# Performance work log

Measured on AMD Instinct MI355X. Metric: run time of the kernel, lower is better.

Reference implementation:

```python
import jax, jax.numpy as jnp
import numpy as np

DIM_MODEL = 1024
NUM_HEADS = 16
DROPOUT_P = 0.5
SCALE = float(np.sqrt(DIM_MODEL // NUM_HEADS))  # NOTE: source MULTIPLIES by this (unusual but faithful)
DROP_KEY = jax.random.key(42)


def setup_inputs() -> dict:
    key = jax.random.key(0)
    ks = jax.random.split(key, 9)
    B, LQ, LK, D = 4, 2048, 2048, DIM_MODEL
    s = 1.0 / np.sqrt(D)
    return {
        "query": jax.random.normal(ks[0], (B, LQ, D), jnp.float32),
        "key": jax.random.normal(ks[1], (B, LK, D), jnp.float32),
        "value": jax.random.normal(ks[2], (B, LK, D), jnp.float32),
        "Wq": jax.random.normal(ks[3], (D, D), jnp.float32) * s,
        "bq": jax.random.normal(ks[4], (D,), jnp.float32) * s,
        "Wk": jax.random.normal(ks[5], (D, D), jnp.float32) * s,
        "bk": jax.random.normal(ks[6], (D,), jnp.float32) * s,
        "Wv": jax.random.normal(ks[7], (D, D), jnp.float32) * s,
        "bv": jax.random.normal(ks[8], (D,), jnp.float32) * s,
    }


def reference(query, key, value, Wq, bq, Wk, bk, Wv, bv):
    # Linear projections (W stored as [in, out])
    q = jnp.einsum('bqd,de->bqe', query, Wq) + bq
    k = jnp.einsum('bkd,de->bke', key, Wk) + bk
    v = jnp.einsum('bkd,de->bke', value, Wv) + bv
    # scores scaled by MULTIPLYING sqrt(d_head), per source
    scores = jnp.einsum('bqe,bke->bqk', q, k) * SCALE
    probs = jax.nn.softmax(scores, axis=-1)
    # dropout (train mode, p=0.5), deterministic fixed key for reproducibility
    keep = jax.random.bernoulli(DROP_KEY, 1.0 - DROPOUT_P, probs.shape)
    probs = jnp.where(keep, probs / (1.0 - DROPOUT_P), 0.0)
    return jnp.einsum('bqk,bke->bqe', probs, v)
```

## Files before the change

### kernel.cpp

```cpp
#include <hip/hip_runtime.h>
#include <math.h>

#define BATCH  4
#define LSEQ   2048
#define DMODEL 1024
#define MROWS  (BATCH * LSEQ)
#define SCORE_SCALE 8.0f

#define THREEFRY_PARTITIONABLE 1

typedef __bf16 bf16_t;
typedef bf16_t bf16x8 __attribute__((ext_vector_type(8)));
typedef bf16_t bf16x4 __attribute__((ext_vector_type(4)));
typedef float  f32x4  __attribute__((ext_vector_type(4)));

#define LDSP(p) ((__attribute__((address_space(3))) void*)(p))
#define GLBP(p) ((const __attribute__((address_space(1))) void*)(p))

__device__ __forceinline__ unsigned rotl32(unsigned x, int r) {
    return (x << r) | (x >> (32 - r));
}

__device__ __forceinline__ void threefry2x32(unsigned k0, unsigned k1,
                                             unsigned x0, unsigned x1,
                                             unsigned& o0, unsigned& o1) {
    const unsigned ks0 = k0, ks1 = k1, ks2 = k0 ^ k1 ^ 0x1BD11BDAu;
    x0 += ks0; x1 += ks1;
#define TF_R(r) { x0 += x1; x1 = rotl32(x1, r); x1 ^= x0; }
    TF_R(13) TF_R(15) TF_R(26) TF_R(6)
    x0 += ks1; x1 += ks2 + 1u;
    TF_R(17) TF_R(29) TF_R(16) TF_R(24)
    x0 += ks2; x1 += ks0 + 2u;
    TF_R(13) TF_R(15) TF_R(26) TF_R(6)
    x0 += ks0; x1 += ks1 + 3u;
    TF_R(17) TF_R(29) TF_R(16) TF_R(24)
    x0 += ks1; x1 += ks2 + 4u;
    TF_R(13) TF_R(15) TF_R(26) TF_R(6)
    x0 += ks2; x1 += ks0 + 5u;
#undef TF_R
    o0 = x0; o1 = x1;
}

__device__ __forceinline__ bool dropout_keep(unsigned n) {
    unsigned o0, o1;
#if THREEFRY_PARTITIONABLE
    threefry2x32(0u, 42u, 0u, n, o0, o1);
    unsigned bits = o0 ^ o1;
#else
    const unsigned HALF = (unsigned)(BATCH * LSEQ) * (unsigned)LSEQ / 2u;
    unsigned c0 = (n < HALF) ? n : (n - HALF);
    unsigned c1 = (n < HALF) ? (n + HALF) : n;
    threefry2x32(0u, 42u, c0, c1, o0, o1);
    unsigned bits = (n < HALF) ? o0 : o1;
#endif
    return bits < 0x80000000u;
}

__global__ __launch_bounds__(256)
void split_f32(const float* __restrict__ X0, const float* __restrict__ X1,
               bf16_t* __restrict__ hi, bf16_t* __restrict__ lo, int n) {
    const int y = blockIdx.y;
    const float* X = y ? X1 : X0;
    long long i = (long long)(blockIdx.x * 256 + threadIdx.x) * 4;
    if (i >= n) return;
    float4 v = *(const float4*)(X + i);
    bf16x4 h, l;
    h[0] = (bf16_t)v.x; l[0] = (bf16_t)(v.x - (float)h[0]);
    h[1] = (bf16_t)v.y; l[1] = (bf16_t)(v.y - (float)h[1]);
    h[2] = (bf16_t)v.z; l[2] = (bf16_t)(v.z - (float)h[2]);
    h[3] = (bf16_t)v.w; l[3] = (bf16_t)(v.w - (float)h[3]);
    *(bf16x4*)(hi + (long long)y * n + i) = h;
    *(bf16x4*)(lo + (long long)y * n + i) = l;
}

__global__ __launch_bounds__(256)
void cvt_bf16(const float* __restrict__ X, bf16_t* __restrict__ Y, int n) {
    long long i = (long long)(blockIdx.x * 256 + threadIdx.x) * 8;
    if (i >= n) return;
    float4 a = *(const float4*)(X + i);
    float4 b = *(const float4*)(X + i + 4);
    bf16x8 o;
    o[0] = (bf16_t)a.x; o[1] = (bf16_t)a.y; o[2] = (bf16_t)a.z; o[3] = (bf16_t)a.w;
    o[4] = (bf16_t)b.x; o[5] = (bf16_t)b.y; o[6] = (bf16_t)b.z; o[7] = (bf16_t)b.w;
    *(bf16x8*)(Y + i) = o;
}

__global__ __launch_bounds__(256)
void split_transpose(const float* __restrict__ W0, const float* __restrict__ W1,
                     bf16_t* __restrict__ Th, bf16_t* __restrict__ Tl,
                     int Kd, int Nd) {
    __shared__ float t[32][33];
    const int z = blockIdx.z;
    const float* W = z ? W1 : W0;
    const long long zo = (long long)z * Kd * Nd;
    const int bx = blockIdx.x * 32;
    const int by = blockIdx.y * 32;
    const int tx = threadIdx.x & 31, ty = threadIdx.x >> 5;
#pragma unroll
    for (int i = 0; i < 4; ++i)
        t[ty + i * 8][tx] = W[(long long)(by + ty + i * 8) * Nd + bx + tx];
    __syncthreads();
#pragma unroll
    for (int i = 0; i < 4; ++i) {
        float v = t[tx][ty + i * 8];
        long long idx = zo + (long long)(bx + ty + i * 8) * Kd + by + tx;
        bf16_t h = (bf16_t)v;
        Th[idx] = h;
        Tl[idx] = (bf16_t)(v - (float)h);
    }
}

template <int OUT>
__global__ __launch_bounds__(512, 2)
void gemm_pipe(const bf16_t* __restrict__ A, const bf16_t* __restrict__ B,
               const float* __restrict__ bias,
               float* __restrict__ Cf, bf16_t* __restrict__ Ch,
               int M, int N, int K, float scale,
               long long sA, long long sB, long long sC,
               int NYt, int NZ) {
    constexpr int ABUF = 128 * 32;
    constexpr int BUFE = ABUF + 256 * 32;
    __shared__ __align__(16) bf16_t smem[3 * BUFE];

    const int bid = blockIdx.x;
    const int gid = (bid & 7) * 32 + (bid >> 3);
    const int nzy = NZ * NYt;
    const int nx = gid / nzy;
    const int rem = gid - nx * nzy;
    const int zz = rem / NYt;
    const int my = rem - zz * NYt;
    const long long z = zz;
    const int m0 = my * 128, n0 = nx * 256;

    const int tid = threadIdx.x;
    const int lane = tid & 63;
    const int wave = tid >> 6;
    const int quad = lane >> 4;
    const int l16 = lane & 15;
    const int wm = (wave >> 2) * 64;
    const int wn = (wave & 3) * 64;

    const bf16_t* gA = A + z * sA;
    const bf16_t* gB = B + z * sB;

    const int lrow = lane >> 2;
    const int scol = ((lane & 3) ^ ((lrow >> 1) & 3)) * 8;
    const int sw = (l16 >> 1) & 3;

    auto stage_tile = [&](int k0, bf16_t* base) {
        {
            const int row = (wave << 4) + lrow;
            __builtin_amdgcn_global_load_lds(
                GLBP(gA + (long long)(m0 + row) * K + k0 + scol),
                LDSP(base + row * 32), 16, 0, 0);
        }
#pragma unroll
        for (int r = 0; r < 2; ++r) {
            const int row = (r << 7) + (wave << 4) + lrow;
            __builtin_amdgcn_global_load_lds(
                GLBP(gB + (long long)(n0 + row) * K + k0 + scol),
                LDSP(base + ABUF + row * 32), 16, 0, 0);
        }
    };

    f32x4 acc[4][4];
#pragma unroll
    for (int i = 0; i < 4; ++i)
#pragma unroll
        for (int j = 0; j < 4; ++j)
            acc[i][j] = (f32x4){0.f, 0.f, 0.f, 0.f};

    bf16x8 fa0[4], fb0[4], fa1[4], fb1[4];

    const int NIT = K >> 5;

    bf16_t* p0 = smem;
    bf16_t* p1 = smem + BUFE;
    bf16_t* p2 = smem + 2 * BUFE;

    stage_tile(0, p0);
    stage_tile(32, p1);
    stage_tile(64, p2);
    asm volatile("s_waitcnt vmcnt(3)" ::: "memory");
    asm volatile("s_barrier" ::: "memory");
    __builtin_amdgcn_sched_barrier(0);
#pragma unroll
    for (int i = 0; i < 4; ++i) {
        const int ao = (wm + i * 16 + l16) * 32 + (quad ^ sw) * 8;
        fa0[i] = *(const bf16x8*)(p0 + ao);
    }
#pragma unroll
    for (int j = 0; j < 4; ++j) {
        const int bo = ABUF + (wn + j * 16 + l16) * 32 + (quad ^ sw) * 8;
        fb0[j] = *(const bf16x8*)(p0 + bo);
    }

#define PIPE_ITER(T, FAc, FBc, FAn, FBn)                                      \
    {                                                                         \
        const int t_ = (T);                                                   \
        if (t_ + 1 < NIT) {                                                   \
            _Pragma("unroll")                                                 \
            for (int i = 0; i < 4; ++i) {                                     \
                const int ao = (wm + i * 16 + l16) * 32 + (quad ^ sw) * 8;    \
                FAn[i] = *(const bf16x8*)(p1 + ao);                           \
            }                                                                 \
            _Pragma("unroll")                                                 \
            for (int j = 0; j < 4; ++j) {                                     \
                const int bo = ABUF + (wn + j * 16 + l16) * 32 + (quad ^ sw) * 8; \
                FBn[j] = *(const bf16x8*)(p1 + bo);                           \
            }                                                                 \
        }                                                                     \
        if (t_ + 3 < NIT) stage_tile((t_ + 3) << 5, p0);                      \
        __builtin_amdgcn_s_setprio(1);                                        \
        _Pragma("unroll")                                                     \
        for (int i = 0; i < 4; ++i)                                           \
            _Pragma("unroll")                                                 \
            for (int j = 0; j < 4; ++j)                                       \
                acc[i][j] = __builtin_amdgcn_mfma_f32_16x16x32_bf16(          \
                    FAc[i], FBc[j], acc[i][j], 0, 0, 0);                      \
        __builtin_amdgcn_s_setprio(0);                                        \
        if (t_ + 2 < NIT) {                                                   \
            asm volatile("s_waitcnt lgkmcnt(0)" ::: "memory");                \
            if (t_ + 3 < NIT) asm volatile("s_waitcnt vmcnt(3)" ::: "memory");\
            else              asm volatile("s_waitcnt vmcnt(0)" ::: "memory");\
            asm volatile("s_barrier" ::: "memory");                           \
            __builtin_amdgcn_sched_barrier(0);                                \
        }                                                                     \
        { bf16_t* tmp_ = p0; p0 = p1; p1 = p2; p2 = tmp_; }                   \
    }

    for (int tp = 0; tp < NIT; tp += 2) {
        PIPE_ITER(tp,     fa0, fb0, fa1, fb1)
        PIPE_ITER(tp + 1, fa1, fb1, fa0, fb0)
    }
#undef PIPE_ITER

#pragma unroll
    for (int i = 0; i < 4; ++i)
#pragma unroll
        for (int j = 0; j < 4; ++j) {
            const int n = n0 + wn + j * 16 + l16;
#pragma unroll
            for (int r = 0; r < 4; ++r) {
                const int m = m0 + wm + i * 16 + quad * 4 + r;
                const long long idx = z * sC + (long long)m * N + n;
                float v = acc[i][j][r];
                if constexpr (OUT == 0) {
                    Cf[idx] = v * scale;
                } else {
                    Ch[idx] = (bf16_t)(v + bias[m]);
                }
            }
        }
}

template <int OUT>
__global__ __launch_bounds__(512, 2)
void gemm_mfma_8ph(const bf16_t* __restrict__ Ah, const bf16_t* __restrict__ Al,
                   const bf16_t* __restrict__ Bh, const bf16_t* __restrict__ Bl,
                   const float* __restrict__ bias, const float* __restrict__ bias2,
                   float* __restrict__ Cf, bf16_t* __restrict__ Ch,
                   bf16_t* __restrict__ Cl,
                   int M, int N, int K, float scale,
                   long long sA, long long sB, long long sC,
                   int NYt, int NZ) {
    constexpr int TM = 256, TN = 256;
    constexpr int PLANE = 256 * 32;
    constexpr int HB = 4 * PLANE;
    __shared__ __align__(16) bf16_t smem[2 * HB];

    const int bid = blockIdx.x;
    const int gid = (bid & 7) * 32 + (bid >> 3);
    const int nzy = NZ * NYt;
    const int nx = gid / nzy;
    const int rem = gid - nx * nzy;
    const int zz = rem / NYt;
    const int my = rem - zz * NYt;
    const long long z = zz;
    const int m0 = my * TM, n0 = nx * TN;

    const int tid = threadIdx.x;
    const int lane = tid & 63;
    const int wave = tid >> 6;
    const int quad = lane >> 4;
    const int l16 = lane & 15;
    const int wm = (wave >> 2) * 128;
    const int wn = (wave & 3) * 64;

    const bf16_t* gAh = Ah + z * sA;
    const bf16_t* gAl = Al + z * sA;
    const bf16_t* gBh = Bh + z * sB;
    const bf16_t* gBl = Bl + z * sB;

    const int lrow = lane >> 2;
    const int scol = ((lane & 3) ^ ((lrow >> 1) & 3)) * 8;
    const int sw = (l16 >> 1) & 3;

    auto stage_round = [&](int r, int k0, bf16_t* base) {
        if (r < 4) {
            const int row = ((r & 1) << 7) + (wave << 4) + lrow;
            const bf16_t* src = (r >= 2) ? gBl : gBh;
            bf16_t* dst = base + ((r >= 2) ? 3 : 2) * PLANE + row * 32;
            __builtin_amdgcn_global_load_lds(
                GLBP(src + (long long)(n0 + row) * K + k0 + scol), LDSP(dst), 16, 0, 0);
        } else {
            const int p = r - 4;
            const int row = (p << 5) + ((wave & 2) ? 128 : 0) + ((wave & 1) << 4) + lrow;
            const bf16_t* src = (wave >= 4) ? gAl : gAh;
            bf16_t* dst = base + ((wave >= 4) ? 1 : 0) * PLANE + row * 32;
            __builtin_amdgcn_global_load_lds(
                GLBP(src + (long long)(m0 + row) * K + k0 + scol), LDSP(dst), 16, 0, 0);
        }
    };

    f32x4 acc[8][4];
#pragma unroll
    for (int i = 0; i < 8; ++i)
#pragma unroll
        for (int j = 0; j < 4; ++j)
            acc[i][j] = (f32x4){0.f, 0.f, 0.f, 0.f};

    bf16x8 ah[2][2], al[2][2];
    bf16x8 bfh[4], bfl[4];

#pragma unroll
    for (int r = 0; r < 8; ++r) stage_round(r, 0, smem);
    asm volatile("s_waitcnt vmcnt(2)" ::: "memory");
    asm volatile("s_barrier" ::: "memory");
    __builtin_amdgcn_sched_barrier(0);
#pragma unroll
    for (int i = 0; i < 2; ++i) {
        const int ao = (wm + i * 16 + l16) * 32 + (quad ^ sw) * 8;
        ah[0][i] = *(const bf16x8*)(smem + ao);
        al[0][i] = *(const bf16x8*)(smem + PLANE + ao);
    }
#pragma unroll
    for (int j = 0; j < 4; ++j) {
        const int bo = (wn + j * 16 + l16) * 32 + (quad ^ sw) * 8;
        bfh[j] = *(const bf16x8*)(smem + 2 * PLANE + bo);
        bfl[j] = *(const bf16x8*)(smem + 3 * PLANE + bo);
    }

    const int NIT = K >> 5;
    for (int itp = 0; itp < NIT; itp += 2) {
#pragma unroll
        for (int h = 0; h < 2; ++h) {
            const int it = itp + h;
            const bool more = (it + 1) < NIT;
            const int k1 = (it + 1) << 5;
            bf16_t* cur = smem + h * HB;
            bf16_t* nxt = smem + (h ^ 1) * HB;
#pragma unroll
            for (int ph = 0; ph < 4; ++ph) {
                if (ph < 3) {
#pragma unroll
                    for (int i = 0; i < 2; ++i) {
                        const int ao = (wm + ((ph + 1) * 2 + i) * 16 + l16) * 32 + (quad ^ sw) * 8;
                        ah[(ph + 1) & 1][i] = *(const bf16x8*)(cur + ao);
                        al[(ph + 1) & 1][i] = *(const bf16x8*)(cur + PLANE + ao);
                    }
                } else if (more) {
#pragma unroll
                    for (int i = 0; i < 2; ++i) {
                        const int ao = (wm + i * 16 + l16) * 32 + (quad ^ sw) * 8;
                        ah[0][i] = *(const bf16x8*)(nxt + ao);
                        al[0][i] = *(const bf16x8*)(nxt + PLANE + ao);
                    }
                }
                if (more) {
                    if (ph == 0)      { stage_round(0, k1, nxt); stage_round(1, k1, nxt); stage_round(2, k1, nxt); }
                    else if (ph == 1) { stage_round(3, k1, nxt); stage_round(4, k1, nxt); }
                    else if (ph == 2) { stage_round(5, k1, nxt); stage_round(6, k1, nxt); }
                    else              { stage_round(7, k1, nxt); }
                }
                __builtin_amdgcn_s_setprio(1);
#pragma unroll
                for (int i = 0; i < 2; ++i)
#pragma unroll
                    for (int j = 0; j < 4; ++j) {
                        f32x4 a = acc[ph * 2 + i][j];
                        a = __builtin_amdgcn_mfma_f32_16x16x32_bf16(ah[ph & 1][i], bfh[j], a, 0, 0, 0);
                        a = __builtin_amdgcn_mfma_f32_16x16x32_bf16(ah[ph & 1][i], bfl[j], a, 0, 0, 0);
                        a = __builtin_amdgcn_mfma_f32_16x16x32_bf16(al[ph & 1][i], bfh[j], a, 0, 0, 0);
                        acc[ph * 2 + i][j] = a;
                    }
                __builtin_amdgcn_s_setprio(0);
                if (ph == 3 && more) {
#pragma unroll
                    for (int j = 0; j < 4; ++j) {
                        const int bo = (wn + j * 16 + l16) * 32 + (quad ^ sw) * 8;
                        bfh[j] = *(const bf16x8*)(nxt + 2 * PLANE + bo);
                        bfl[j] = *(const bf16x8*)(nxt + 3 * PLANE + bo);
                    }
                }
                if (more) {
                    if (ph == 0)      asm volatile("s_waitcnt vmcnt(4)" ::: "memory");
                    else if (ph == 1) asm volatile("s_waitcnt vmcnt(5)" ::: "memory");
                    else              asm volatile("s_waitcnt vmcnt(2)" ::: "memory");
                    asm volatile("s_barrier" ::: "memory");
                    __builtin_amdgcn_sched_barrier(0);
                } else {
                    if (ph == 0) {
                        asm volatile("s_waitcnt vmcnt(1)" ::: "memory");
                        asm volatile("s_barrier" ::: "memory");
                        __builtin_amdgcn_sched_barrier(0);
                    } else if (ph == 1) {
                        asm volatile("s_waitcnt vmcnt(0)" ::: "memory");
                        asm volatile("s_barrier" ::: "memory");
                        __builtin_amdgcn_sched_barrier(0);
                    }
                }
            }
        }
    }

    const float* bz = (z == 1 && bias2) ? bias2 : bias;
#pragma unroll
    for (int i = 0; i < 8; ++i)
#pragma unroll
        for (int j = 0; j < 4; ++j) {
            const int n = n0 + wn + j * 16 + l16;
            float bvn = 0.f;
            if constexpr (OUT != 0) bvn = bz[n];
#pragma unroll
            for (int r = 0; r < 4; ++r) {
                const int m = m0 + wm + i * 16 + quad * 4 + r;
                const long long idx = z * sC + (long long)m * N + n;
                float v = acc[i][j][r];
                if constexpr (OUT == 0) {
                    Cf[idx] = v * scale;
                } else {
                    v += bvn;
                    bf16_t h = (bf16_t)v;
                    Ch[idx] = h;
                    Cl[idx] = (bf16_t)(v - (float)h);
                }
            }
        }
}

__global__ __launch_bounds__(256)
void softmax_dropout(const float* __restrict__ S, bf16_t* __restrict__ P) {
    const unsigned row = blockIdx.x;
    const float* rp = S + (long long)row * LSEQ;
    const int tid = threadIdx.x;

    float v[8];
    *(float4*)(v)     = *(const float4*)(rp + tid * 8);
    *(float4*)(v + 4) = *(const float4*)(rp + tid * 8 + 4);

    float m = v[0];
#pragma unroll
    for (int e = 1; e < 8; ++e) m = fmaxf(m, v[e]);
#pragma unroll
    for (int o = 1; o < 64; o <<= 1) m = fmaxf(m, __shfl_xor(m, o));
    __shared__ float redm[4];
    if ((tid & 63) == 0) redm[tid >> 6] = m;
    __syncthreads();
    m = fmaxf(fmaxf(redm[0], redm[1]), fmaxf(redm[2], redm[3]));

    float s = 0.f;
#pragma unroll
    for (int e = 0; e < 8; ++e) { v[e] = __expf(v[e] - m); s += v[e]; }
#pragma unroll
    for (int o = 1; o < 64; o <<= 1) s += __shfl_xor(s, o);
    __shared__ float reds[4];
    if ((tid & 63) == 0) reds[tid >> 6] = s;
    __syncthreads();
    s = (reds[0] + reds[1]) + (reds[2] + reds[3]);

    const float inv = 2.0f / s;
    const unsigned nb = row * (unsigned)LSEQ + (unsigned)(tid * 8);
    bf16x8 o8;
#pragma unroll
    for (int e = 0; e < 8; ++e)
        o8[e] = (bf16_t)(dropout_keep(nb + e) ? v[e] * inv : 0.0f);
    *(bf16x8*)(P + (long long)row * LSEQ + tid * 8) = o8;
}

extern "C" void kernel_launch(void* const* d_in, const int* in_sizes, int n_in,
                              void* d_out, int out_size, void* d_ws, size_t ws_size,
                              hipStream_t stream) {
    const float* query = (const float*)d_in[0];
    const float* key_  = (const float*)d_in[1];
    const float* value = (const float*)d_in[2];
    const float* Wq = (const float*)d_in[3];
    const float* bq = (const float*)d_in[4];
    const float* Wk = (const float*)d_in[5];
    const float* bk = (const float*)d_in[6];
    const float* Wv = (const float*)d_in[7];
    const float* bv = (const float*)d_in[8];
    float* out = (float*)d_out;

    char* w = (char*)d_ws;
    const size_t Q1 = (size_t)MROWS * DMODEL * 2;
    bf16_t* Qh  = (bf16_t*)(w);
    bf16_t* Ql  = (bf16_t*)(w + 2 * Q1);
    bf16_t* VT  = (bf16_t*)(w + 4 * Q1);
    float*  S   = (float*)(w + 5 * Q1);
    bf16_t* XvH  = (bf16_t*)(w + 5 * Q1);
    bf16_t* XqkH = (bf16_t*)(w + 5 * Q1);
    bf16_t* XqkL = (bf16_t*)(w + 7 * Q1);
    bf16_t* WTh = (bf16_t*)(w + 9 * Q1);
    bf16_t* WTl = (bf16_t*)(w + 9 * Q1 + 2 * (size_t)DMODEL * DMODEL * 2);
    bf16_t* P   = Qh;

    dim3 b256(256);
    dim3 b512(512);
    const int NELEM = MROWS * DMODEL;
    const long long DD = (long long)DMODEL * DMODEL;
    dim3 gwt1(DMODEL / 32, DMODEL / 32, 1);
    dim3 gwt2(DMODEL / 32, DMODEL / 32, 2);

    split_transpose<<<gwt1, b256, 0, stream>>>(Wv, nullptr, WTh, WTl, DMODEL, DMODEL);
    cvt_bf16<<<dim3(NELEM / 2048), b256, 0, stream>>>(value, XvH, NELEM);
    gemm_pipe<2><<<dim3(256), b512, 0, stream>>>(
        WTh, XvH, bv, nullptr, VT,
        DMODEL, LSEQ, DMODEL, 1.f,
        0, (long long)LSEQ * DMODEL, (long long)DMODEL * LSEQ,
        DMODEL / 128, 4);

    split_transpose<<<gwt2, b256, 0, stream>>>(Wq, Wk, WTh, WTl, DMODEL, DMODEL);
    split_f32<<<dim3(NELEM / 1024, 2), b256, 0, stream>>>(query, key_, XqkH, XqkL, NELEM);
    gemm_mfma_8ph<1><<<dim3(256), b512, 0, stream>>>(
        XqkH, XqkL, WTh, WTl, bq, bk, nullptr, Qh, Ql,
        MROWS, DMODEL, DMODEL, 1.f,
        (long long)NELEM, DD, (long long)NELEM,
        MROWS / 256, 2);

    gemm_mfma_8ph<0><<<dim3(256), b512, 0, stream>>>(
        Qh, Ql, Qh + NELEM, Ql + NELEM, nullptr, nullptr, S, nullptr, nullptr,
        LSEQ, LSEQ, DMODEL, SCORE_SCALE,
        (long long)LSEQ * DMODEL, (long long)LSEQ * DMODEL,
        (long long)LSEQ * LSEQ,
        LSEQ / 256, 4);

    softmax_dropout<<<dim3(MROWS), b256, 0, stream>>>(S, P);

    gemm_pipe<0><<<dim3(256), b512, 0, stream>>>(
        P, VT, nullptr, out, nullptr,
        LSEQ, DMODEL, LSEQ, 1.f,
        (long long)LSEQ * LSEQ, (long long)DMODEL * LSEQ, (long long)LSEQ * DMODEL,
        LSEQ / 128, 4);
}
```

Baseline: 425.1 us.

## Stage GEMM epilogues through LDS for vectorized stores and merge prep kernels

GEMM epilogues now write each wave's accumulator tile into a swizzled LDS strip, then read it back as rows so global stores are 4-wide contiguous vectors instead of scattered scalar stores. This targets the uncoalesced writes of the large S score matrix and of the Q/K hi/lo outputs. Separately, the weight split/transpose and input conversion kernels for Q, K and V are fused into two launches, which requires rearranging workspace buffers so they do not alias. The fused launches add an extra LDS round trip and barrier per epilogue and bring a risk of buffer overlap errors.

```diff
diff --git a/kernel.cpp b/kernel.cpp
--- a/kernel.cpp
+++ b/kernel.cpp
@@ -57,10 +57,12 @@
 }
 
 __global__ __launch_bounds__(256)
-void split_f32(const float* __restrict__ X0, const float* __restrict__ X1,
-               bf16_t* __restrict__ hi, bf16_t* __restrict__ lo, int n) {
+void split_all(const float* __restrict__ Xq, const float* __restrict__ Xk,
+               const float* __restrict__ Xv,
+               bf16_t* __restrict__ hi, bf16_t* __restrict__ lo,
+               bf16_t* __restrict__ vh, int n) {
     const int y = blockIdx.y;
-    const float* X = y ? X1 : X0;
+    const float* X = (y == 0) ? Xq : (y == 1) ? Xk : Xv;
     long long i = (long long)(blockIdx.x * 256 + threadIdx.x) * 4;
     if (i >= n) return;
     float4 v = *(const float4*)(X + i);
@@ -69,30 +71,25 @@
     h[1] = (bf16_t)v.y; l[1] = (bf16_t)(v.y - (float)h[1]);
     h[2] = (bf16_t)v.z; l[2] = (bf16_t)(v.z - (float)h[2]);
     h[3] = (bf16_t)v.w; l[3] = (bf16_t)(v.w - (float)h[3]);
-    *(bf16x4*)(hi + (long long)y * n + i) = h;
-    *(bf16x4*)(lo + (long long)y * n + i) = l;
+    if (y < 2) {
+        *(bf16x4*)(hi + (long long)y * n + i) = h;
+        *(bf16x4*)(lo + (long long)y * n + i) = l;
+    } else {
+        *(bf16x4*)(vh + i) = h;
+    }
 }
 
 __global__ __launch_bounds__(256)
-void cvt_bf16(const float* __restrict__ X, bf16_t* __restrict__ Y, int n) {
-    long long i = (long long)(blockIdx.x * 256 + threadIdx.x) * 8;
-    if (i >= n) return;
-    float4 a = *(const float4*)(X + i);
-    float4 b = *(const float4*)(X + i + 4);
-    bf16x8 o;
-    o[0] = (bf16_t)a.x; o[1] = (bf16_t)a.y; o[2] = (bf16_t)a.z; o[3] = (bf16_t)a.w;
-    o[4] = (bf16_t)b.x; o[5] = (bf16_t)b.y; o[6] = (bf16_t)b.z; o[7] = (bf16_t)b.w;
-    *(bf16x8*)(Y + i) = o;
-}
-
-__global__ __launch_bounds__(256)
-void split_transpose(const float* __restrict__ W0, const float* __restrict__ W1,
-                     bf16_t* __restrict__ Th, bf16_t* __restrict__ Tl,
-                     int Kd, int Nd) {
+void split_transpose3(const float* __restrict__ W0, const float* __restrict__ W1,
+                      const float* __restrict__ W2,
+                      bf16_t* __restrict__ Th01, bf16_t* __restrict__ Tl01,
+                      bf16_t* __restrict__ Thv, bf16_t* __restrict__ Tlv,
+                      int Kd, int Nd) {
     __shared__ float t[32][33];
     const int z = blockIdx.z;
-    const float* W = z ? W1 : W0;
-    const long long zo = (long long)z * Kd * Nd;
+    const float* W = (z == 0) ? W0 : (z == 1) ? W1 : W2;
+    bf16_t* Th = (z == 2) ? Thv : Th01 + (long long)z * Kd * Nd;
+    bf16_t* Tl = (z == 2) ? Tlv : Tl01 + (long long)z * Kd * Nd;
     const int bx = blockIdx.x * 32;
     const int by = blockIdx.y * 32;
     const int tx = threadIdx.x & 31, ty = threadIdx.x >> 5;
@@ -103,7 +100,7 @@
 #pragma unroll
     for (int i = 0; i < 4; ++i) {
         float v = t[tx][ty + i * 8];
-        long long idx = zo + (long long)(bx + ty + i * 8) * Kd + by + tx;
+        long long idx = (long long)(bx + ty + i * 8) * Kd + by + tx;
         bf16_t h = (bf16_t)v;
         Th[idx] = h;
         Tl[idx] = (bf16_t)(v - (float)h);
@@ -235,23 +232,43 @@
     }
 #undef PIPE_ITER
 
-#pragma unroll
-    for (int i = 0; i < 4; ++i)
-#pragma unroll
-        for (int j = 0; j < 4; ++j) {
-            const int n = n0 + wn + j * 16 + l16;
+    asm volatile("s_barrier" ::: "memory");
+    float* strip = (float*)smem + wave * 1024;
+#pragma unroll
+    for (int i = 0; i < 4; ++i) {
+#pragma unroll
+        for (int j = 0; j < 4; ++j)
 #pragma unroll
             for (int r = 0; r < 4; ++r) {
-                const int m = m0 + wm + i * 16 + quad * 4 + r;
-                const long long idx = z * sC + (long long)m * N + n;
-                float v = acc[i][j][r];
-                if constexpr (OUT == 0) {
-                    Cf[idx] = v * scale;
-                } else {
-                    Ch[idx] = (bf16_t)(v + bias[m]);
-                }
+                const int row = quad * 4 + r;
+                const int col = j * 16 + l16;
+                strip[row * 64 + (col ^ (row << 2))] = acc[i][j][r];
+            }
+        asm volatile("s_waitcnt lgkmcnt(0)" ::: "memory");
+        __builtin_amdgcn_sched_barrier(0);
+#pragma unroll
+        for (int k = 0; k < 4; ++k) {
+            const int R = k * 4 + (lane >> 4);
+            const int c = (lane & 15) * 4;
+            f32x4 v = *(const f32x4*)(strip + R * 64 + (c ^ (R << 2)));
+            const int grow = m0 + wm + i * 16 + R;
+            const int gcol = n0 + wn + c;
+            const long long idx = z * sC + (long long)grow * N + gcol;
+            if constexpr (OUT == 0) {
+                v *= scale;
+                *(f32x4*)(Cf + idx) = v;
+            } else {
+                const float bm = bias[grow];
+                v += bm;
+                bf16x4 h4;
+                h4[0] = (bf16_t)v[0]; h4[1] = (bf16_t)v[1];
+                h4[2] = (bf16_t)v[2]; h4[3] = (bf16_t)v[3];
+                *(bf16x4*)(Ch + idx) = h4;
             }
         }
+        asm volatile("s_waitcnt lgkmcnt(0)" ::: "memory");
+        __builtin_amdgcn_sched_barrier(0);
+    }
 }
 
 template <int OUT>
@@ -414,29 +431,48 @@
         }
     }
 
+    asm volatile("s_barrier" ::: "memory");
+    float* strip = (float*)smem + wave * 1024;
     const float* bz = (z == 1 && bias2) ? bias2 : bias;
 #pragma unroll
-    for (int i = 0; i < 8; ++i)
-#pragma unroll
-        for (int j = 0; j < 4; ++j) {
-            const int n = n0 + wn + j * 16 + l16;
-            float bvn = 0.f;
-            if constexpr (OUT != 0) bvn = bz[n];
+    for (int i = 0; i < 8; ++i) {
+#pragma unroll
+        for (int j = 0; j < 4; ++j)
 #pragma unroll
             for (int r = 0; r < 4; ++r) {
-                const int m = m0 + wm + i * 16 + quad * 4 + r;
-                const long long idx = z * sC + (long long)m * N + n;
-                float v = acc[i][j][r];
-                if constexpr (OUT == 0) {
-                    Cf[idx] = v * scale;
-                } else {
-                    v += bvn;
-                    bf16_t h = (bf16_t)v;
-                    Ch[idx] = h;
-                    Cl[idx] = (bf16_t)(v - (float)h);
+                const int row = quad * 4 + r;
+                const int col = j * 16 + l16;
+                strip[row * 64 + (col ^ (row << 2))] = acc[i][j][r];
+            }
+        asm volatile("s_waitcnt lgkmcnt(0)" ::: "memory");
+        __builtin_amdgcn_sched_barrier(0);
+#pragma unroll
+        for (int k = 0; k < 4; ++k) {
+            const int R = k * 4 + (lane >> 4);
+            const int c = (lane & 15) * 4;
+            f32x4 v = *(const f32x4*)(strip + R * 64 + (c ^ (R << 2)));
+            const int grow = m0 + wm + i * 16 + R;
+            const int gcol = n0 + wn + c;
+            const long long idx = z * sC + (long long)grow * N + gcol;
+            if constexpr (OUT == 0) {
+                v *= scale;
+                *(f32x4*)(Cf + idx) = v;
+            } else {
+                f32x4 b4 = *(const f32x4*)(bz + gcol);
+                v += b4;
+                bf16x4 h4, l4;
+#pragma unroll
+                for (int e = 0; e < 4; ++e) {
+                    h4[e] = (bf16_t)v[e];
+                    l4[e] = (bf16_t)(v[e] - (float)h4[e]);
                 }
+                *(bf16x4*)(Ch + idx) = h4;
+                *(bf16x4*)(Cl + idx) = l4;
             }
         }
+        asm volatile("s_waitcnt lgkmcnt(0)" ::: "memory");
+        __builtin_amdgcn_sched_barrier(0);
+    }
 }
 
 __global__ __launch_bounds__(256)
@@ -494,11 +530,14 @@
 
     char* w = (char*)d_ws;
     const size_t Q1 = (size_t)MROWS * DMODEL * 2;
+    const long long DD = (long long)DMODEL * DMODEL;
     bf16_t* Qh  = (bf16_t*)(w);
     bf16_t* Ql  = (bf16_t*)(w + 2 * Q1);
     bf16_t* VT  = (bf16_t*)(w + 4 * Q1);
     float*  S   = (float*)(w + 5 * Q1);
-    bf16_t* XvH  = (bf16_t*)(w + 5 * Q1);
+    bf16_t* XvH  = (bf16_t*)(w);
+    bf16_t* WvTh = (bf16_t*)(w + 2 * Q1);
+    bf16_t* WvTl = WvTh + DD;
     bf16_t* XqkH = (bf16_t*)(w + 5 * Q1);
     bf16_t* XqkL = (bf16_t*)(w + 7 * Q1);
     bf16_t* WTh = (bf16_t*)(w + 9 * Q1);
@@ -508,20 +547,18 @@
     dim3 b256(256);
     dim3 b512(512);
     const int NELEM = MROWS * DMODEL;
-    const long long DD = (long long)DMODEL * DMODEL;
-    dim3 gwt1(DMODEL / 32, DMODEL / 32, 1);
-    dim3 gwt2(DMODEL / 32, DMODEL / 32, 2);
-
-    split_transpose<<<gwt1, b256, 0, stream>>>(Wv, nullptr, WTh, WTl, DMODEL, DMODEL);
-    cvt_bf16<<<dim3(NELEM / 2048), b256, 0, stream>>>(value, XvH, NELEM);
+
+    split_transpose3<<<dim3(DMODEL / 32, DMODEL / 32, 3), b256, 0, stream>>>(
+        Wq, Wk, Wv, WTh, WTl, WvTh, WvTl, DMODEL, DMODEL);
+    split_all<<<dim3(NELEM / 1024, 3), b256, 0, stream>>>(
+        query, key_, value, XqkH, XqkL, XvH, NELEM);
+
     gemm_pipe<2><<<dim3(256), b512, 0, stream>>>(
-        WTh, XvH, bv, nullptr, VT,
+        WvTh, XvH, bv, nullptr, VT,
         DMODEL, LSEQ, DMODEL, 1.f,
         0, (long long)LSEQ * DMODEL, (long long)DMODEL * LSEQ,
         DMODEL / 128, 4);
 
-    split_transpose<<<gwt2, b256, 0, stream>>>(Wq, Wk, WTh, WTl, DMODEL, DMODEL);
-    split_f32<<<dim3(NELEM / 1024, 2), b256, 0, stream>>>(query, key_, XqkH, XqkL, NELEM);
     gemm_mfma_8ph<1><<<dim3(256), b512, 0, stream>>>(
         XqkH, XqkL, WTh, WTl, bq, bk, nullptr, Qh, Ql,
         MROWS, DMODEL, DMODEL, 1.f,
```

Result: no change. 428.0 us (+0.7%).
